# Kernel tuning notes

Measured on AMD Instinct MI355X. Metric: run time of the kernel, lower is better.

## Reference

```python
import jax, jax.numpy as jnp
import numpy as np

B_, C_, H_, W_ = 4, 512, 64, 64

def setup_inputs() -> dict:
    key = jax.random.key(0)
    kx, kb, kc, kd, kg = jax.random.split(key, 5)
    scale = 1.0 / np.sqrt(C_)
    x = jax.random.normal(kx, (B_, C_, H_, W_), dtype=jnp.float32)
    Wb = jax.random.normal(kb, (C_, C_), dtype=jnp.float32) * scale
    Wc = jax.random.normal(kc, (C_, C_), dtype=jnp.float32) * scale
    Wd = jax.random.normal(kd, (C_, C_), dtype=jnp.float32) * scale
    gamma = jax.random.normal(kg, (1,), dtype=jnp.float32) * 0.1
    return {"x": x, "Wb": Wb, "Wc": Wc, "Wd": Wd, "gamma": gamma}

def reference(x, Wb, Wc, Wd, gamma):
    b, c, h, w = x.shape
    n = h * w
    xf = x.reshape(b, c, n)                       # (b, c, N)
    # 1x1 convs (bias=False) == per-pixel channel matmuls
    Bm = jnp.einsum('oc,bcn->bon', Wb, xf)        # (b, c, N)
    Cm = jnp.einsum('oc,bcn->bon', Wc, xf)
    Dm = jnp.einsum('oc,bcn->bon', Wd, xf)
    # S = softmax(B^T C, axis=2): (b, N, N), no scaling (faithful to source)
    S = jax.nn.softmax(jnp.einsum('bcn,bcm->bnm', Bm, Cm), axis=-1)
    # attention_maps = D @ S^T : (b, c, N)
    att = jnp.einsum('bcm,bnm->bcn', Dm, S).reshape(b, c, h, w)
    return gamma * att + x
```

## Files before the change

### kernel.cpp

```cpp
#include <hip/hip_runtime.h>
#include <math.h>
#include <stdint.h>

#define CC 512
#define NN 4096
#define BB 4

typedef _Float16 f16;
typedef _Float16 f16x8 __attribute__((ext_vector_type(8)));
typedef _Float16 f16x4 __attribute__((ext_vector_type(4)));
typedef float f32x4 __attribute__((ext_vector_type(4)));

__device__ __forceinline__ void gload_lds16(const void* g, void* l) {
    __builtin_amdgcn_global_load_lds(
        (const __attribute__((address_space(1))) void*)g,
        (__attribute__((address_space(3))) void*)l, 16, 0, 0);
}

template<int ROWS>
__device__ __forceinline__ void stage_tile(const f16* __restrict__ g, int stride_e,
                                           f16* lds, int wid, int lane) {
    constexpr int ITERS = ROWS * 8 / 64 / 4;
    #pragma unroll
    for (int it = 0; it < ITERS; ++it) {
        int flatbase = (wid * ITERS + it) * 64;
        f16* dst = lds + flatbase * 8;
        int flat = flatbase + lane;
        int r = flat >> 3, c = flat & 7;
        const f16* src = g + (size_t)r * stride_e + ((c ^ (r & 7)) << 3);
        gload_lds16(src, dst);
    }
}

__device__ __forceinline__ f16x8 frag_ld(const f16* lds, int r, int ch) {
    return *(const f16x8*)(lds + r * 64 + ((ch ^ (r & 7)) << 3));
}

#define MFMA16(a, b, c) __builtin_amdgcn_mfma_f32_16x16x32_f16((a), (b), (c), 0, 0, 0)

template<int N>
__device__ __forceinline__ float ror16(float x) {
    return __int_as_float(__builtin_amdgcn_update_dpp(
        0, __float_as_int(x), 0x120 + N, 0xF, 0xF, true));
}
__device__ __forceinline__ f32x4 rmax16(f32x4 v) {
    #pragma unroll
    for (int q = 0; q < 4; ++q) {
        float x = v[q];
        x = fmaxf(x, ror16<1>(x));
        x = fmaxf(x, ror16<2>(x));
        x = fmaxf(x, ror16<4>(x));
        x = fmaxf(x, ror16<8>(x));
        v[q] = x;
    }
    return v;
}
__device__ __forceinline__ f32x4 rsum16(f32x4 v) {
    #pragma unroll
    for (int q = 0; q < 4; ++q) {
        float x = v[q];
        x += ror16<1>(x);
        x += ror16<2>(x);
        x += ror16<4>(x);
        x += ror16<8>(x);
        v[q] = x;
    }
    return v;
}

__global__ __launch_bounds__(256) void wcvt_k(const float* __restrict__ Wb,
                                              const float* __restrict__ Wc,
                                              const float* __restrict__ Wd,
                                              f16* __restrict__ W16) {
    int i = blockIdx.x * 256 + threadIdx.x;
    int idx = i * 4;
    int m = idx >> 18;
    int off = idx & 262143;
    const float* src = (m == 0) ? Wb : (m == 1) ? Wc : Wd;
    f32x4 v = *(const f32x4*)(src + off);
    f16x4 h = { (f16)v[0], (f16)v[1], (f16)v[2], (f16)v[3] };
    *(f16x4*)(W16 + idx) = h;
}

__global__ __launch_bounds__(256) void proj_k(const float* __restrict__ x,
                                              const f16* __restrict__ W16,
                                              f16* __restrict__ Bt, f16* __restrict__ Ct,
                                              f16* __restrict__ Dm) {
    const int wsel = blockIdx.z % 3;
    const int b = blockIdx.z / 3;
    const f16* __restrict__ W = W16 + (size_t)wsel * CC * CC;
    const float* __restrict__ X = x + (size_t)b * CC * NN;
    const size_t p16 = (size_t)CC * NN;
    const int o0 = blockIdx.y * 128, n0 = blockIdx.x * 128;

    __shared__ __align__(16) char smraw[34816];
    f16* As = (f16*)smraw;
    f16* Bs = As + 128 * 64;
    f16* T  = (f16*)smraw;

    const int t = threadIdx.x;
    const int wid = t >> 6, lane = t & 63;
    const int wr = wid >> 1, wc = wid & 1;

    f32x4 acc[4][4] = {};
    const int cg = t & 7;
    const int n4 = ((t >> 3) & 31) * 4;

    for (int kc = 0; kc < CC; kc += 64) {
        __syncthreads();
        stage_tile<128>(W + (size_t)o0 * CC + kc, CC, As, wid, lane);
        f32x4 v[8];
        #pragma unroll
        for (int i = 0; i < 8; ++i)
            v[i] = *(const f32x4*)(X + (size_t)(kc + cg * 8 + i) * NN + n0 + n4);
        #pragma unroll
        for (int j = 0; j < 4; ++j) {
            f16x8 h = { (f16)v[0][j], (f16)v[1][j], (f16)v[2][j], (f16)v[3][j],
                        (f16)v[4][j], (f16)v[5][j], (f16)v[6][j], (f16)v[7][j] };
            int r = n4 + j;
            *(f16x8*)(Bs + r * 64 + ((cg ^ (r & 7)) << 3)) = h;
        }
        __syncthreads();
        #pragma unroll
        for (int ks = 0; ks < 2; ++ks) {
            int ch = ks * 4 + (lane >> 4);
            f16x8 a[4], bb[4];
            #pragma unroll
            for (int i = 0; i < 4; ++i) a[i]  = frag_ld(As, wr * 64 + i * 16 + (lane & 15), ch);
            #pragma unroll
            for (int j = 0; j < 4; ++j) bb[j] = frag_ld(Bs, wc * 64 + j * 16 + (lane & 15), ch);
            #pragma unroll
            for (int i = 0; i < 4; ++i)
                #pragma unroll
                for (int j = 0; j < 4; ++j)
                    acc[i][j] = MFMA16(a[i], bb[j], acc[i][j]);
        }
    }

    __syncthreads();
    if (wsel < 2) {
        #pragma unroll
        for (int i = 0; i < 4; ++i)
            #pragma unroll
            for (int j = 0; j < 4; ++j) {
                int n_l = wc * 64 + j * 16 + (lane & 15);
                int o_l = wr * 64 + i * 16 + (lane >> 4) * 4;
                f16x4 h = { (f16)acc[i][j][0], (f16)acc[i][j][1], (f16)acc[i][j][2], (f16)acc[i][j][3] };
                *(f16x4*)(T + n_l * 136 + o_l) = h;
            }
        __syncthreads();
        f16* __restrict__ dst = ((wsel == 0) ? Bt : Ct) + (size_t)b * p16;
        int n = t & 127;
        #pragma unroll
        for (int it = 0; it < 8; ++it) {
            int ch8 = (t >> 7) * 8 + it;
            f16x8 h = *(f16x8*)(T + n * 136 + ch8 * 8);
            *(f16x8*)(dst + (size_t)(n0 + n) * CC + o0 + ch8 * 8) = h;
        }
    } else {
        #pragma unroll
        for (int i = 0; i < 4; ++i)
            #pragma unroll
            for (int j = 0; j < 4; ++j) {
                int n_l = wc * 64 + j * 16 + (lane & 15);
                #pragma unroll
                for (int q = 0; q < 4; ++q) {
                    int o_l = wr * 64 + i * 16 + (lane >> 4) * 4 + q;
                    T[o_l * 136 + n_l] = (f16)acc[i][j][q];
                }
            }
        __syncthreads();
        f16* __restrict__ dst = Dm + (size_t)b * p16;
        int o = t & 127;
        #pragma unroll
        for (int it = 0; it < 8; ++it) {
            int ch8 = (t >> 7) * 8 + it;
            f16x8 h = *(f16x8*)(T + o * 136 + ch8 * 8);
            *(f16x8*)(dst + (size_t)(o0 + o) * NN + n0 + ch8 * 8) = h;
        }
    }
}

__device__ __forceinline__ void stage_Ct32(const f16* __restrict__ Ctb, f16* dstbase,
                                           int m0, int w4, int lane) {
    #pragma unroll
    for (int it = 0; it < 8; ++it) {
        int flatbase = (w4 * 8 + it) * 64;
        f16* dst = dstbase + flatbase * 8;
        int r = flatbase >> 6;
        const f16* src = Ctb + (size_t)(m0 + r) * CC + ((lane ^ (r & 7)) << 3);
        gload_lds16(src, dst);
    }
}
__device__ __forceinline__ void stage_Dt32(const f16* __restrict__ Dmb, f16* DtB,
                                           int m0, int w4, int lane) {
    #pragma unroll
    for (int it = 0; it < 8; ++it) {
        int flatbase = (w4 * 8 + it) * 64;
        f16* dst = DtB + flatbase * 8;
        int flat = flatbase + lane;
        int r = flat >> 2, c4 = flat & 3;
        const f16* src = Dmb + (size_t)r * NN + m0 + (c4 << 3);
        gload_lds16(src, dst);
    }
}

__global__ __launch_bounds__(512) void flash_k(
    const float* __restrict__ x, const float* __restrict__ gamma_p,
    const f16* __restrict__ Bt, const f16* __restrict__ Ct,
    const f16* __restrict__ Dm, float* __restrict__ out)
{
    __shared__ __align__(16) char sm[139776];
    f16*   CtB  = (f16*)sm;
    f16*   DtB  = (f16*)(sm + 65536);
    f16*   PSB  = (f16*)(sm + 98304);
    float* SCL  = (float*)(sm + 106496);
    float* LROW = (float*)(sm + 139264);

    const int bx = blockIdx.x;
    const int j8 = bx & 7;
    const int b = j8 >> 1;
    const int n0 = ((bx >> 3) + (j8 & 1) * 32) * 64;

    const size_t p16 = (size_t)CC * NN;
    const f16* __restrict__ Btb = Bt + (size_t)b * p16;
    const f16* __restrict__ Ctb = Ct + (size_t)b * p16;
    const f16* __restrict__ Dmb = Dm + (size_t)b * p16;

    const int t = threadIdx.x;
    const int wid = t >> 6, lane = t & 63;
    const int w4 = wid & 3;
    const bool isP = wid < 4;
    const int l15 = lane & 15, g = lane >> 4;

    f32x4 R[32];
    f32x4 m_run = (f32x4)(-INFINITY);
    f32x4 l_run = (f32x4)(0.f);

    if (isP) {
        const f16* qrow = Btb + (size_t)(n0 + w4 * 16 + l15) * CC + g * 8;
        #pragma unroll
        for (int s = 0; s < 16; ++s)
            R[s] = __builtin_bit_cast(f32x4, *(const f16x8*)(qrow + s * 32));
    } else {
        #pragma unroll
        for (int i = 0; i < 32; ++i) R[i] = (f32x4)(0.f);
    }

    if (isP) stage_Ct32(Ctb, CtB, 0, w4, lane);
    __syncthreads();

    for (int i = 0; i < 128; ++i) {
        const int cur = i & 1;
        if (isP) {
            if (i + 1 < 128) stage_Ct32(Ctb, CtB + (cur ^ 1) * 16384, (i + 1) * 32, w4, lane);
            f32x4 S0 = (f32x4)(0.f), S1 = (f32x4)(0.f);
            const f16* cb = CtB + cur * 16384;
            __builtin_amdgcn_s_setprio(1);
            #pragma unroll
            for (int s = 0; s < 16; ++s) {
                int ch = s * 4 + g;
                f16x8 b0 = *(const f16x8*)(cb + l15 * 512 + ((ch ^ (l15 & 7)) << 3));
                f16x8 b1 = *(const f16x8*)(cb + (16 + l15) * 512 + ((ch ^ (l15 & 7)) << 3));
                f16x8 q = __builtin_bit_cast(f16x8, R[s]);
                S0 = MFMA16(q, b0, S0);
                S1 = MFMA16(q, b1, S1);
            }
            __builtin_amdgcn_s_setprio(0);
            f32x4 tm, scl;
            #pragma unroll
            for (int q = 0; q < 4; ++q) tm[q] = fmaxf(S0[q], S1[q]);
            tm = rmax16(tm);
            #pragma unroll
            for (int q = 0; q < 4; ++q) {
                float mnew = fmaxf(m_run[q], tm[q]);
                scl[q] = __expf(m_run[q] - mnew);
                m_run[q] = mnew;
                S0[q] = __expf(S0[q] - mnew);
                S1[q] = __expf(S1[q] - mnew);
            }
            f32x4 ps;
            #pragma unroll
            for (int q = 0; q < 4; ++q) ps[q] = S0[q] + S1[q];
            ps = rsum16(ps);
            #pragma unroll
            for (int q = 0; q < 4; ++q) l_run[q] = l_run[q] * scl[q] + ps[q];
            if (l15 == 0) *(f32x4*)(SCL + cur * 64 + w4 * 16 + g * 4) = scl;
            f16* pp = PSB + cur * 2048;
            #pragma unroll
            for (int q = 0; q < 4; ++q) {
                int row = w4 * 16 + g * 4 + q;
                pp[row * 32 + ((((l15 >> 3) ^ g) << 3) | (l15 & 7))] = (f16)S0[q];
                pp[row * 32 + ((((2 + (l15 >> 3)) ^ g) << 3) | (l15 & 7))] = (f16)S1[q];
            }
        } else {
            if (i > 0) {
                const int prev = cur ^ 1;
                const f16* pp = PSB + prev * 2048;
                const float* sc = SCL + prev * 64;
                f32x4 scl4[4];
                #pragma unroll
                for (int na = 0; na < 4; ++na)
                    scl4[na] = *(const f32x4*)(sc + na * 16 + g * 4);
                #pragma unroll
                for (int na = 0; na < 4; ++na)
                    #pragma unroll
                    for (int cb = 0; cb < 8; ++cb)
                        #pragma unroll
                        for (int q = 0; q < 4; ++q)
                            R[na * 8 + cb][q] *= scl4[na][q];
                f16x8 pa[4];
                #pragma unroll
                for (int na = 0; na < 4; ++na) {
                    int row = na * 16 + l15;
                    pa[na] = *(const f16x8*)(pp + row * 32 + ((g ^ (l15 >> 2)) << 3));
                }
                f16x8 d[8];
                #pragma unroll
                for (int cb = 0; cb < 8; ++cb)
                    d[cb] = *(const f16x8*)(DtB + (w4 * 128 + cb * 16 + l15) * 32 + (g << 3));
                __builtin_amdgcn_s_setprio(1);
                #pragma unroll
                for (int na = 0; na < 4; ++na)
                    #pragma unroll
                    for (int cb = 0; cb < 8; ++cb)
                        R[na * 8 + cb] = MFMA16(pa[na], d[cb], R[na * 8 + cb]);
                __builtin_amdgcn_s_setprio(0);
                __builtin_amdgcn_sched_barrier(0);
            }
            stage_Dt32(Dmb, DtB, i * 32, w4, lane);
        }
        __syncthreads();
    }

    if (isP) {
        if (l15 == 0) *(f32x4*)(LROW + w4 * 16 + g * 4) = l_run;
    } else {
        const f16* pp = PSB + 2048;
        const float* sc = SCL + 64;
        f32x4 scl4[4];
        #pragma unroll
        for (int na = 0; na < 4; ++na)
            scl4[na] = *(const f32x4*)(sc + na * 16 + g * 4);
        #pragma unroll
        for (int na = 0; na < 4; ++na)
            #pragma unroll
            for (int cb = 0; cb < 8; ++cb)
                #pragma unroll
                for (int q = 0; q < 4; ++q)
                    R[na * 8 + cb][q] *= scl4[na][q];
        f16x8 pa[4];
        #pragma unroll
        for (int na = 0; na < 4; ++na) {
            int row = na * 16 + l15;
            pa[na] = *(const f16x8*)(pp + row * 32 + ((g ^ (l15 >> 2)) << 3));
        }
        f16x8 d[8];
        #pragma unroll
        for (int cb = 0; cb < 8; ++cb)
            d[cb] = *(const f16x8*)(DtB + (w4 * 128 + cb * 16 + l15) * 32 + (g << 3));
        #pragma unroll
        for (int na = 0; na < 4; ++na)
            #pragma unroll
            for (int cb = 0; cb < 8; ++cb)
                R[na * 8 + cb] = MFMA16(pa[na], d[cb], R[na * 8 + cb]);
    }
    __syncthreads();

    const float gam = gamma_p[0];
    float* T = (float*)sm;
    if (!isP) {
        #pragma unroll
        for (int na = 0; na < 4; ++na) {
            f32x4 lr = *(const f32x4*)(LROW + na * 16 + g * 4);
            f32x4 inv;
            #pragma unroll
            for (int q = 0; q < 4; ++q) inv[q] = gam / lr[q];
            #pragma unroll
            for (int cb = 0; cb < 8; ++cb) {
                int c = w4 * 128 + cb * 16 + l15;
                f32x4 v;
                #pragma unroll
                for (int q = 0; q < 4; ++q) v[q] = R[na * 8 + cb][q] * inv[q];
                *(f32x4*)(T + c * 68 + na * 16 + g * 4) = v;
            }
        }
    }
    __syncthreads();

    const float* __restrict__ xb = x + (size_t)b * CC * NN;
    float* __restrict__ ob = out + (size_t)b * CC * NN;
    #pragma unroll
    for (int it = 0; it < 16; ++it) {
        int c = (t >> 4) + it * 32;
        int n4 = (t & 15) * 4;
        f32x4 v = *(const f32x4*)(T + c * 68 + n4);
        f32x4 xv = *(const f32x4*)(xb + (size_t)c * NN + n0 + n4);
        #pragma unroll
        for (int q = 0; q < 4; ++q) v[q] += xv[q];
        *(f32x4*)(ob + (size_t)c * NN + n0 + n4) = v;
    }
}

extern "C" void kernel_launch(void* const* d_in, const int* in_sizes, int n_in,
                              void* d_out, int out_size, void* d_ws, size_t ws_size,
                              hipStream_t stream) {
    const float* x  = (const float*)d_in[0];
    const float* Wb = (const float*)d_in[1];
    const float* Wc = (const float*)d_in[2];
    const float* Wd = (const float*)d_in[3];
    const float* gm = (const float*)d_in[4];
    float* out = (float*)d_out;
    char* ws = (char*)d_ws;

    f16* W16 = (f16*)(ws);
    f16* Bt  = (f16*)(ws + 1572864);
    f16* Ct  = (f16*)(ws + 1572864 + 16777216);
    f16* Dm  = (f16*)(ws + 1572864 + 2 * 16777216);

    wcvt_k<<<dim3(768), 256, 0, stream>>>(Wb, Wc, Wd, W16);
    proj_k<<<dim3(32, 4, 12), 256, 0, stream>>>(x, W16, Bt, Ct, Dm);
    flash_k<<<dim3(256), 512, 0, stream>>>(x, gm, Bt, Ct, Dm, out);
}
```

Baseline: 369.2 us.

## Split flash kernel into producer, softmax and PV warp roles with lazy rescale

Warps are regrouped into three roles: two warps compute QK^T and softmax for 32 rows each, four warps run the P·V MFMAs, and two dedicated loader warps stage both the C and D tiles into double-buffered LDS. The loop now runs one extra iteration so the PV stage trails by one step, with D also double-buffered. The online-softmax max is only updated when a new row max exceeds the running max by more than 8, and a flag lets the PV warps skip the accumulator rescale otherwise. This moves global loads off the compute warps and removes most rescale work, but it concentrates softmax on fewer warps and lets un-normalised exponentials grow up to e^8 before being stored in f16.

After: 551.0 us. 49.2% more time.

```diff
diff --git a/kernel.cpp b/kernel.cpp
--- a/kernel.cpp
+++ b/kernel.cpp
@@ -181,41 +181,18 @@
     }
 }
 
-__device__ __forceinline__ void stage_Ct32(const f16* __restrict__ Ctb, f16* dstbase,
-                                           int m0, int w4, int lane) {
-    #pragma unroll
-    for (int it = 0; it < 8; ++it) {
-        int flatbase = (w4 * 8 + it) * 64;
-        f16* dst = dstbase + flatbase * 8;
-        int r = flatbase >> 6;
-        const f16* src = Ctb + (size_t)(m0 + r) * CC + ((lane ^ (r & 7)) << 3);
-        gload_lds16(src, dst);
-    }
-}
-__device__ __forceinline__ void stage_Dt32(const f16* __restrict__ Dmb, f16* DtB,
-                                           int m0, int w4, int lane) {
-    #pragma unroll
-    for (int it = 0; it < 8; ++it) {
-        int flatbase = (w4 * 8 + it) * 64;
-        f16* dst = DtB + flatbase * 8;
-        int flat = flatbase + lane;
-        int r = flat >> 2, c4 = flat & 3;
-        const f16* src = Dmb + (size_t)r * NN + m0 + (c4 << 3);
-        gload_lds16(src, dst);
-    }
-}
-
 __global__ __launch_bounds__(512) void flash_k(
     const float* __restrict__ x, const float* __restrict__ gamma_p,
     const f16* __restrict__ Bt, const f16* __restrict__ Ct,
     const f16* __restrict__ Dm, float* __restrict__ out)
 {
-    __shared__ __align__(16) char sm[139776];
+    __shared__ __align__(16) char sm[140064];
     f16*   CtB  = (f16*)sm;
     f16*   DtB  = (f16*)(sm + 65536);
-    f16*   PSB  = (f16*)(sm + 98304);
-    float* SCL  = (float*)(sm + 106496);
-    float* LROW = (float*)(sm + 139264);
+    f16*   PSB  = (f16*)(sm + 131072);
+    float* SCL  = (float*)(sm + 139264);
+    int*   FLG  = (int*)(sm + 139776);
+    float* LROW = (float*)(sm + 139792);
 
     const int bx = blockIdx.x;
     const int j8 = bx & 7;
@@ -229,96 +206,140 @@
 
     const int t = threadIdx.x;
     const int wid = t >> 6, lane = t & 63;
-    const int w4 = wid & 3;
-    const bool isP = wid < 4;
     const int l15 = lane & 15, g = lane >> 4;
 
     f32x4 R[32];
-    f32x4 m_run = (f32x4)(-INFINITY);
-    f32x4 l_run = (f32x4)(0.f);
-
-    if (isP) {
-        const f16* qrow = Btb + (size_t)(n0 + w4 * 16 + l15) * CC + g * 8;
-        #pragma unroll
-        for (int s = 0; s < 16; ++s)
-            R[s] = __builtin_bit_cast(f32x4, *(const f16x8*)(qrow + s * 32));
+    f32x4 m_run0 = (f32x4)(-INFINITY), m_run1 = (f32x4)(-INFINITY);
+    f32x4 l_run0 = (f32x4)(0.f), l_run1 = (f32x4)(0.f);
+
+    if (wid < 2) {
+        const f16* q0 = Btb + (size_t)(n0 + wid * 32 + l15) * CC + g * 8;
+        const f16* q1 = q0 + (size_t)16 * CC;
+        #pragma unroll
+        for (int s = 0; s < 16; ++s) {
+            R[s]      = __builtin_bit_cast(f32x4, *(const f16x8*)(q0 + s * 32));
+            R[16 + s] = __builtin_bit_cast(f32x4, *(const f16x8*)(q1 + s * 32));
+        }
     } else {
         #pragma unroll
         for (int i = 0; i < 32; ++i) R[i] = (f32x4)(0.f);
     }
 
-    if (isP) stage_Ct32(Ctb, CtB, 0, w4, lane);
+    if (wid >= 6) {
+        const int u = wid - 6;
+        #pragma unroll
+        for (int it = 0; it < 16; ++it) {
+            int r = u * 16 + it;
+            gload_lds16(Ctb + (size_t)r * CC + ((lane ^ (r & 7)) << 3), CtB + r * 512);
+        }
+    }
     __syncthreads();
 
-    for (int i = 0; i < 128; ++i) {
+    for (int i = 0; i <= 128; ++i) {
         const int cur = i & 1;
-        if (isP) {
-            if (i + 1 < 128) stage_Ct32(Ctb, CtB + (cur ^ 1) * 16384, (i + 1) * 32, w4, lane);
-            f32x4 S0 = (f32x4)(0.f), S1 = (f32x4)(0.f);
-            const f16* cb = CtB + cur * 16384;
-            __builtin_amdgcn_s_setprio(1);
-            #pragma unroll
-            for (int s = 0; s < 16; ++s) {
-                int ch = s * 4 + g;
-                f16x8 b0 = *(const f16x8*)(cb + l15 * 512 + ((ch ^ (l15 & 7)) << 3));
-                f16x8 b1 = *(const f16x8*)(cb + (16 + l15) * 512 + ((ch ^ (l15 & 7)) << 3));
-                f16x8 q = __builtin_bit_cast(f16x8, R[s]);
-                S0 = MFMA16(q, b0, S0);
-                S1 = MFMA16(q, b1, S1);
-            }
-            __builtin_amdgcn_s_setprio(0);
-            f32x4 tm, scl;
-            #pragma unroll
-            for (int q = 0; q < 4; ++q) tm[q] = fmaxf(S0[q], S1[q]);
-            tm = rmax16(tm);
-            #pragma unroll
-            for (int q = 0; q < 4; ++q) {
-                float mnew = fmaxf(m_run[q], tm[q]);
-                scl[q] = __expf(m_run[q] - mnew);
-                m_run[q] = mnew;
-                S0[q] = __expf(S0[q] - mnew);
-                S1[q] = __expf(S1[q] - mnew);
-            }
-            f32x4 ps;
-            #pragma unroll
-            for (int q = 0; q < 4; ++q) ps[q] = S0[q] + S1[q];
-            ps = rsum16(ps);
-            #pragma unroll
-            for (int q = 0; q < 4; ++q) l_run[q] = l_run[q] * scl[q] + ps[q];
-            if (l15 == 0) *(f32x4*)(SCL + cur * 64 + w4 * 16 + g * 4) = scl;
-            f16* pp = PSB + cur * 2048;
-            #pragma unroll
-            for (int q = 0; q < 4; ++q) {
-                int row = w4 * 16 + g * 4 + q;
-                pp[row * 32 + ((((l15 >> 3) ^ g) << 3) | (l15 & 7))] = (f16)S0[q];
-                pp[row * 32 + ((((2 + (l15 >> 3)) ^ g) << 3) | (l15 & 7))] = (f16)S1[q];
-            }
-        } else {
+        if (wid < 2) {
+            if (i < 128) {
+                const int p = wid;
+                const f16* cb = CtB + cur * 16384;
+                f32x4 S00 = (f32x4)(0.f), S01 = (f32x4)(0.f);
+                f32x4 S10 = (f32x4)(0.f), S11 = (f32x4)(0.f);
+                const int off7 = l15 & 7;
+                __builtin_amdgcn_s_setprio(1);
+                #pragma unroll
+                for (int s = 0; s < 16; ++s) {
+                    int sw = (((s * 4 + g) ^ off7) << 3);
+                    f16x8 b0 = *(const f16x8*)(cb + l15 * 512 + sw);
+                    f16x8 b1 = *(const f16x8*)(cb + (16 + l15) * 512 + sw);
+                    f16x8 qa = __builtin_bit_cast(f16x8, R[s]);
+                    f16x8 qb = __builtin_bit_cast(f16x8, R[16 + s]);
+                    S00 = MFMA16(qa, b0, S00); S01 = MFMA16(qa, b1, S01);
+                    S10 = MFMA16(qb, b0, S10); S11 = MFMA16(qb, b1, S11);
+                }
+                __builtin_amdgcn_s_setprio(0);
+                f32x4 tm0, tm1;
+                #pragma unroll
+                for (int q = 0; q < 4; ++q) {
+                    tm0[q] = fmaxf(S00[q], S01[q]);
+                    tm1[q] = fmaxf(S10[q], S11[q]);
+                }
+                tm0 = rmax16(tm0); tm1 = rmax16(tm1);
+                int grow = 0;
+                #pragma unroll
+                for (int q = 0; q < 4; ++q)
+                    grow |= (tm0[q] > m_run0[q] + 8.f) | (tm1[q] > m_run1[q] + 8.f);
+                const bool doR = __any(grow);
+                f32x4 scl0 = (f32x4)(1.f), scl1 = (f32x4)(1.f);
+                if (doR) {
+                    #pragma unroll
+                    for (int q = 0; q < 4; ++q) {
+                        float mn = fmaxf(m_run0[q], tm0[q]);
+                        scl0[q] = __expf(m_run0[q] - mn); m_run0[q] = mn;
+                        mn = fmaxf(m_run1[q], tm1[q]);
+                        scl1[q] = __expf(m_run1[q] - mn); m_run1[q] = mn;
+                    }
+                }
+                #pragma unroll
+                for (int q = 0; q < 4; ++q) {
+                    S00[q] = __expf(S00[q] - m_run0[q]);
+                    S01[q] = __expf(S01[q] - m_run0[q]);
+                    S10[q] = __expf(S10[q] - m_run1[q]);
+                    S11[q] = __expf(S11[q] - m_run1[q]);
+                }
+                f32x4 ps0, ps1;
+                #pragma unroll
+                for (int q = 0; q < 4; ++q) { ps0[q] = S00[q] + S01[q]; ps1[q] = S10[q] + S11[q]; }
+                ps0 = rsum16(ps0); ps1 = rsum16(ps1);
+                #pragma unroll
+                for (int q = 0; q < 4; ++q) {
+                    l_run0[q] = l_run0[q] * scl0[q] + ps0[q];
+                    l_run1[q] = l_run1[q] * scl1[q] + ps1[q];
+                }
+                if (l15 == 0) {
+                    *(f32x4*)(SCL + cur * 64 + p * 32 + g * 4) = scl0;
+                    *(f32x4*)(SCL + cur * 64 + p * 32 + 16 + g * 4) = scl1;
+                }
+                if (lane == 0) FLG[cur * 2 + p] = doR ? 1 : 0;
+                f16* pp = PSB + cur * 2048;
+                const int posA = (((l15 >> 3) ^ g) << 3);
+                const int posB = (((2 + (l15 >> 3)) ^ g) << 3);
+                const int m7 = l15 & 7;
+                #pragma unroll
+                for (int q = 0; q < 4; ++q) {
+                    int r0 = p * 32 + g * 4 + q;
+                    int r1 = r0 + 16;
+                    pp[r0 * 32 + posA + m7] = (f16)S00[q];
+                    pp[r0 * 32 + posB + m7] = (f16)S01[q];
+                    pp[r1 * 32 + posA + m7] = (f16)S10[q];
+                    pp[r1 * 32 + posB + m7] = (f16)S11[q];
+                }
+            }
+        } else if (wid < 6) {
             if (i > 0) {
+                const int c4 = wid - 2;
                 const int prev = cur ^ 1;
                 const f16* pp = PSB + prev * 2048;
-                const float* sc = SCL + prev * 64;
-                f32x4 scl4[4];
+                int fl = FLG[prev * 2] | FLG[prev * 2 + 1];
+                if (fl) {
+                    #pragma unroll
+                    for (int na = 0; na < 4; ++na) {
+                        f32x4 s4 = *(const f32x4*)(SCL + prev * 64 + na * 16 + g * 4);
+                        #pragma unroll
+                        for (int cb = 0; cb < 8; ++cb)
+                            #pragma unroll
+                            for (int q = 0; q < 4; ++q)
+                                R[na * 8 + cb][q] *= s4[q];
+                    }
+                }
+                f16x8 pa[4];
                 #pragma unroll
                 for (int na = 0; na < 4; ++na)
-                    scl4[na] = *(const f32x4*)(sc + na * 16 + g * 4);
-                #pragma unroll
-                for (int na = 0; na < 4; ++na)
-                    #pragma unroll
-                    for (int cb = 0; cb < 8; ++cb)
-                        #pragma unroll
-                        for (int q = 0; q < 4; ++q)
-                            R[na * 8 + cb][q] *= scl4[na][q];
-                f16x8 pa[4];
-                #pragma unroll
-                for (int na = 0; na < 4; ++na) {
-                    int row = na * 16 + l15;
-                    pa[na] = *(const f16x8*)(pp + row * 32 + ((g ^ (l15 >> 2)) << 3));
-                }
+                    pa[na] = *(const f16x8*)(pp + (na * 16 + l15) * 32 +
+                                             ((g ^ ((l15 >> 2) & 3)) << 3));
                 f16x8 d[8];
                 #pragma unroll
                 for (int cb = 0; cb < 8; ++cb)
-                    d[cb] = *(const f16x8*)(DtB + (w4 * 128 + cb * 16 + l15) * 32 + (g << 3));
+                    d[cb] = *(const f16x8*)(DtB + prev * 16384 +
+                                            (c4 * 128 + cb * 16 + l15) * 32 + (g << 3));
                 __builtin_amdgcn_s_setprio(1);
                 #pragma unroll
                 for (int na = 0; na < 4; ++na)
@@ -326,50 +347,43 @@
                     for (int cb = 0; cb < 8; ++cb)
                         R[na * 8 + cb] = MFMA16(pa[na], d[cb], R[na * 8 + cb]);
                 __builtin_amdgcn_s_setprio(0);
-                __builtin_amdgcn_sched_barrier(0);
-            }
-            stage_Dt32(Dmb, DtB, i * 32, w4, lane);
+            }
+        } else {
+            const int u = wid - 6;
+            if (i + 1 < 128) {
+                f16* db = CtB + (cur ^ 1) * 16384;
+                const int m0n = (i + 1) * 32;
+                #pragma unroll
+                for (int it = 0; it < 16; ++it) {
+                    int r = u * 16 + it;
+                    gload_lds16(Ctb + (size_t)(m0n + r) * CC + ((lane ^ (r & 7)) << 3),
+                                db + r * 512);
+                }
+            }
+            if (i < 128) {
+                f16* dd = DtB + cur * 16384;
+                const int m0c = i * 32;
+                #pragma unroll
+                for (int it = 0; it < 16; ++it) {
+                    int flatbase = (u * 16 + it) * 64;
+                    int flat = flatbase + lane;
+                    int r = flat >> 2, c4m = flat & 3;
+                    gload_lds16(Dmb + (size_t)r * NN + m0c + (c4m << 3), dd + flatbase * 8);
+                }
+            }
         }
         __syncthreads();
     }
 
-    if (isP) {
-        if (l15 == 0) *(f32x4*)(LROW + w4 * 16 + g * 4) = l_run;
-    } else {
-        const f16* pp = PSB + 2048;
-        const float* sc = SCL + 64;
-        f32x4 scl4[4];
-        #pragma unroll
-        for (int na = 0; na < 4; ++na)
-            scl4[na] = *(const f32x4*)(sc + na * 16 + g * 4);
-        #pragma unroll
-        for (int na = 0; na < 4; ++na)
-            #pragma unroll
-            for (int cb = 0; cb < 8; ++cb)
-                #pragma unroll
-                for (int q = 0; q < 4; ++q)
-                    R[na * 8 + cb][q] *= scl4[na][q];
-        f16x8 pa[4];
-        #pragma unroll
-        for (int na = 0; na < 4; ++na) {
-            int row = na * 16 + l15;
-            pa[na] = *(const f16x8*)(pp + row * 32 + ((g ^ (l15 >> 2)) << 3));
-        }
-        f16x8 d[8];
-        #pragma unroll
-        for (int cb = 0; cb < 8; ++cb)
-            d[cb] = *(const f16x8*)(DtB + (w4 * 128 + cb * 16 + l15) * 32 + (g << 3));
-        #pragma unroll
-        for (int na = 0; na < 4; ++na)
-            #pragma unroll
-            for (int cb = 0; cb < 8; ++cb)
-                R[na * 8 + cb] = MFMA16(pa[na], d[cb], R[na * 8 + cb]);
+    if (wid < 2 && l15 == 0) {
+        *(f32x4*)(LROW + wid * 32 + g * 4) = l_run0;
+        *(f32x4*)(LROW + wid * 32 + 16 + g * 4) = l_run1;
     }
     __syncthreads();
-
     const float gam = gamma_p[0];
     float* T = (float*)sm;
-    if (!isP) {
+    if (wid >= 2 && wid < 6) {
+        const int c4 = wid - 2;
         #pragma unroll
         for (int na = 0; na < 4; ++na) {
             f32x4 lr = *(const f32x4*)(LROW + na * 16 + g * 4);
@@ -378,7 +392,7 @@
             for (int q = 0; q < 4; ++q) inv[q] = gam / lr[q];
             #pragma unroll
             for (int cb = 0; cb < 8; ++cb) {
-                int c = w4 * 128 + cb * 16 + l15;
+                int c = c4 * 128 + cb * 16 + l15;
                 f32x4 v;
                 #pragma unroll
                 for (int q = 0; q < 4; ++q) v[q] = R[na * 8 + cb][q] * inv[q];
@@ -387,7 +401,6 @@
         }
     }
     __syncthreads();
-
     const float* __restrict__ xb = x + (size_t)b * CC * NN;
     float* __restrict__ ob = out + (size_t)b * CC * NN;
     #pragma unroll
```

## Double-buffer D tiles and replace syncthreads with manual waitcnt barriers

Applied to the files above, without the earlier changes.

Consumer waves now prefetch the next D tile into a second LDS buffer before doing the current PV MFMA step. They wait with a partial vmcnt so the global load overlaps the matrix math, where before the load was issued after compute and covered by a full barrier. The full __syncthreads is replaced with explicit waitcnt plus s_barrier wrapped in sched_barriers. The epilogue is folded into an extra loop iteration. LDS use grows slightly, and correctness now depends on the hand-written vmcnt counts being exact.

Result: slower. 465.9 us (+26.2%).

```diff
diff --git a/kernel.cpp b/kernel.cpp
--- a/kernel.cpp
+++ b/kernel.cpp
@@ -210,12 +210,12 @@
     const f16* __restrict__ Bt, const f16* __restrict__ Ct,
     const f16* __restrict__ Dm, float* __restrict__ out)
 {
-    __shared__ __align__(16) char sm[139776];
+    __shared__ __align__(16) char sm[140032];
     f16*   CtB  = (f16*)sm;
     f16*   DtB  = (f16*)(sm + 65536);
-    f16*   PSB  = (f16*)(sm + 98304);
-    float* SCL  = (float*)(sm + 106496);
-    float* LROW = (float*)(sm + 139264);
+    f16*   PSB  = (f16*)(sm + 131072);
+    float* SCL  = (float*)(sm + 139264);
+    float* LROW = (float*)(sm + 139776);
 
     const int bx = blockIdx.x;
     const int j8 = bx & 7;
@@ -247,54 +247,68 @@
         for (int i = 0; i < 32; ++i) R[i] = (f32x4)(0.f);
     }
 
-    if (isP) stage_Ct32(Ctb, CtB, 0, w4, lane);
-    __syncthreads();
-
-    for (int i = 0; i < 128; ++i) {
+    if (isP) {
+        stage_Ct32(Ctb, CtB, 0, w4, lane);
+        asm volatile("s_waitcnt vmcnt(0)" ::: "memory");
+    }
+    __builtin_amdgcn_sched_barrier(0);
+    __builtin_amdgcn_s_barrier();
+    __builtin_amdgcn_sched_barrier(0);
+
+    for (int i = 0; i <= 128; ++i) {
         const int cur = i & 1;
         if (isP) {
-            if (i + 1 < 128) stage_Ct32(Ctb, CtB + (cur ^ 1) * 16384, (i + 1) * 32, w4, lane);
-            f32x4 S0 = (f32x4)(0.f), S1 = (f32x4)(0.f);
-            const f16* cb = CtB + cur * 16384;
-            __builtin_amdgcn_s_setprio(1);
-            #pragma unroll
-            for (int s = 0; s < 16; ++s) {
-                int ch = s * 4 + g;
-                f16x8 b0 = *(const f16x8*)(cb + l15 * 512 + ((ch ^ (l15 & 7)) << 3));
-                f16x8 b1 = *(const f16x8*)(cb + (16 + l15) * 512 + ((ch ^ (l15 & 7)) << 3));
-                f16x8 q = __builtin_bit_cast(f16x8, R[s]);
-                S0 = MFMA16(q, b0, S0);
-                S1 = MFMA16(q, b1, S1);
-            }
-            __builtin_amdgcn_s_setprio(0);
-            f32x4 tm, scl;
-            #pragma unroll
-            for (int q = 0; q < 4; ++q) tm[q] = fmaxf(S0[q], S1[q]);
-            tm = rmax16(tm);
-            #pragma unroll
-            for (int q = 0; q < 4; ++q) {
-                float mnew = fmaxf(m_run[q], tm[q]);
-                scl[q] = __expf(m_run[q] - mnew);
-                m_run[q] = mnew;
-                S0[q] = __expf(S0[q] - mnew);
-                S1[q] = __expf(S1[q] - mnew);
-            }
-            f32x4 ps;
-            #pragma unroll
-            for (int q = 0; q < 4; ++q) ps[q] = S0[q] + S1[q];
-            ps = rsum16(ps);
-            #pragma unroll
-            for (int q = 0; q < 4; ++q) l_run[q] = l_run[q] * scl[q] + ps[q];
-            if (l15 == 0) *(f32x4*)(SCL + cur * 64 + w4 * 16 + g * 4) = scl;
-            f16* pp = PSB + cur * 2048;
-            #pragma unroll
-            for (int q = 0; q < 4; ++q) {
-                int row = w4 * 16 + g * 4 + q;
-                pp[row * 32 + ((((l15 >> 3) ^ g) << 3) | (l15 & 7))] = (f16)S0[q];
-                pp[row * 32 + ((((2 + (l15 >> 3)) ^ g) << 3) | (l15 & 7))] = (f16)S1[q];
+            if (i < 128) {
+                if (i + 1 < 128)
+                    stage_Ct32(Ctb, CtB + (cur ^ 1) * 16384, (i + 1) * 32, w4, lane);
+                f32x4 S0 = (f32x4)(0.f), S1 = (f32x4)(0.f);
+                const f16* cb = CtB + cur * 16384;
+                __builtin_amdgcn_s_setprio(1);
+                #pragma unroll
+                for (int s = 0; s < 16; ++s) {
+                    int ch = s * 4 + g;
+                    f16x8 b0 = *(const f16x8*)(cb + l15 * 512 + ((ch ^ (l15 & 7)) << 3));
+                    f16x8 b1 = *(const f16x8*)(cb + (16 + l15) * 512 + ((ch ^ (l15 & 7)) << 3));
+                    f16x8 q = __builtin_bit_cast(f16x8, R[s]);
+                    S0 = MFMA16(q, b0, S0);
+                    S1 = MFMA16(q, b1, S1);
+                }
+                __builtin_amdgcn_s_setprio(0);
+                f32x4 tm, scl;
+                #pragma unroll
+                for (int q = 0; q < 4; ++q) tm[q] = fmaxf(S0[q], S1[q]);
+                tm = rmax16(tm);
+                #pragma unroll
+                for (int q = 0; q < 4; ++q) {
+                    float mnew = fmaxf(m_run[q], tm[q]);
+                    scl[q] = __expf(m_run[q] - mnew);
+                    m_run[q] = mnew;
+                    S0[q] = __expf(S0[q] - mnew);
+                    S1[q] = __expf(S1[q] - mnew);
+                }
+                f32x4 ps;
+                #pragma unroll
+                for (int q = 0; q < 4; ++q) ps[q] = S0[q] + S1[q];
+                ps = rsum16(ps);
+                #pragma unroll
+                for (int q = 0; q < 4; ++q) l_run[q] = l_run[q] * scl[q] + ps[q];
+                if (l15 == 0) *(f32x4*)(SCL + cur * 64 + w4 * 16 + g * 4) = scl;
+                f16* pp = PSB + cur * 2048;
+                #pragma unroll
+                for (int q = 0; q < 4; ++q) {
+                    int row = w4 * 16 + g * 4 + q;
+                    pp[row * 32 + ((((l15 >> 3) ^ g) << 3) | (l15 & 7))] = (f16)S0[q];
+                    pp[row * 32 + ((((2 + (l15 >> 3)) ^ g) << 3) | (l15 & 7))] = (f16)S1[q];
+                }
+                asm volatile("s_waitcnt lgkmcnt(0)" ::: "memory");
+                asm volatile("s_waitcnt vmcnt(0)" ::: "memory");
             }
         } else {
+            if (i < 128) stage_Dt32(Dmb, DtB + cur * 16384, i * 32, w4, lane);
             if (i > 0) {
+                if (i < 128) asm volatile("s_waitcnt vmcnt(8)" ::: "memory");
+                else         asm volatile("s_waitcnt vmcnt(0)" ::: "memory");
+                __builtin_amdgcn_sched_barrier(0);
                 const int prev = cur ^ 1;
                 const f16* pp = PSB + prev * 2048;
                 const float* sc = SCL + prev * 64;
@@ -318,7 +332,8 @@
                 f16x8 d[8];
                 #pragma unroll
                 for (int cb = 0; cb < 8; ++cb)
-                    d[cb] = *(const f16x8*)(DtB + (w4 * 128 + cb * 16 + l15) * 32 + (g << 3));
+                    d[cb] = *(const f16x8*)(DtB + prev * 16384 +
+                                            (w4 * 128 + cb * 16 + l15) * 32 + (g << 3));
                 __builtin_amdgcn_s_setprio(1);
                 #pragma unroll
                 for (int na = 0; na < 4; ++na)
@@ -326,47 +341,15 @@
                     for (int cb = 0; cb < 8; ++cb)
                         R[na * 8 + cb] = MFMA16(pa[na], d[cb], R[na * 8 + cb]);
                 __builtin_amdgcn_s_setprio(0);
-                __builtin_amdgcn_sched_barrier(0);
             }
-            stage_Dt32(Dmb, DtB, i * 32, w4, lane);
-        }
-        __syncthreads();
-    }
-
-    if (isP) {
-        if (l15 == 0) *(f32x4*)(LROW + w4 * 16 + g * 4) = l_run;
-    } else {
-        const f16* pp = PSB + 2048;
-        const float* sc = SCL + 64;
-        f32x4 scl4[4];
-        #pragma unroll
-        for (int na = 0; na < 4; ++na)
-            scl4[na] = *(const f32x4*)(sc + na * 16 + g * 4);
-        #pragma unroll
-        for (int na = 0; na < 4; ++na)
-            #pragma unroll
-            for (int cb = 0; cb < 8; ++cb)
-                #pragma unroll
-                for (int q = 0; q < 4; ++q)
-                    R[na * 8 + cb][q] *= scl4[na][q];
-        f16x8 pa[4];
-        #pragma unroll
-        for (int na = 0; na < 4; ++na) {
-            int row = na * 16 + l15;
-            pa[na] = *(const f16x8*)(pp + row * 32 + ((g ^ (l15 >> 2)) << 3));
-        }
-        f16x8 d[8];
-        #pragma unroll
-        for (int cb = 0; cb < 8; ++cb)
-            d[cb] = *(const f16x8*)(DtB + (w4 * 128 + cb * 16 + l15) * 32 + (g << 3));
-        #pragma unroll
-        for (int na = 0; na < 4; ++na)
-            #pragma unroll
-            for (int cb = 0; cb < 8; ++cb)
-                R[na * 8 + cb] = MFMA16(pa[na], d[cb], R[na * 8 + cb]);
-    }
+        }
+        __builtin_amdgcn_sched_barrier(0);
+        __builtin_amdgcn_s_barrier();
+        __builtin_amdgcn_sched_barrier(0);
+    }
+
+    if (isP && l15 == 0) *(f32x4*)(LROW + w4 * 16 + g * 4) = l_run;
     __syncthreads();
-
     const float gam = gamma_p[0];
     float* T = (float*)sm;
     if (!isP) {
@@ -387,7 +370,6 @@
         }
     }
     __syncthreads();
-
     const float* __restrict__ xb = x + (size_t)b * CC * NN;
     float* __restrict__ ob = out + (size_t)b * CC * NN;
     #pragma unroll
```
